# Kernel tuning notes

Measured on AMD Instinct MI355X. Metric: run time of the kernel, lower is better.

## Reference

```python
import jax, jax.numpy as jnp
import numpy as np
from jax import lax

INT8_NARROW = (-127.0, 127.0)   # brevitas Int8WeightPerTensorFloat (narrow range)
INT8_FULL = (-128.0, 127.0)     # brevitas Int8ActPerTensorFloat
INT32 = (-2.0**31, 2.0**31 - 1)


def _fake_quant(v, scale, qmin, qmax):
    # round-to-nearest, clip, dequant (per-tensor)
    return jnp.clip(jnp.round(v / scale), qmin, qmax) * scale


def _conv(x, w, stride):
    return lax.conv_general_dilated(
        x, w, window_strides=(stride, stride), padding=[(1, 1), (1, 1)],
        dimension_numbers=("NCHW", "OIHW", "NCHW"))


def setup_inputs() -> dict:
    key = jax.random.key(0)
    ks = jax.random.split(key, 5)
    B, Cin, Cout, H = 64, 256, 512, 28
    x = jax.random.normal(ks[0], (B, Cin, H, H), dtype=jnp.float32)
    w1 = jax.random.normal(ks[1], (Cout, Cin, 3, 3), dtype=jnp.float32) * 0.05
    b1 = jax.random.normal(ks[2], (Cout,), dtype=jnp.float32) * 0.01
    w2 = jax.random.normal(ks[3], (Cout, Cout, 3, 3), dtype=jnp.float32) * 0.05
    b2 = jax.random.normal(ks[4], (Cout,), dtype=jnp.float32) * 0.01
    return {
        "x": x, "w1": w1, "b1": b1, "w2": w2, "b2": b2,
        "in_scale": jnp.full((1,), 0.05, dtype=jnp.float32),
        "act1_scale": jnp.full((1,), 0.05, dtype=jnp.float32),
        "act2_scale": jnp.full((1,), 0.05, dtype=jnp.float32),
    }


def reference(x, w1, b1, w2, b2, in_scale, act1_scale, act2_scale):
    s_in = in_scale[0]
    s_a1 = act1_scale[0]
    s_a2 = act2_scale[0]

    # conv1: per-tensor int8 weight fake-quant (max-abs stats, narrow range)
    s_w1 = jnp.max(jnp.abs(w1)) / 127.0
    wq1 = _fake_quant(w1, s_w1, *INT8_NARROW)
    bq1 = _fake_quant(b1, s_in * s_w1, *INT32)  # Int32Bias: scale = in_scale*w_scale
    out = _conv(x, wq1, 2) + bq1[None, :, None, None]

    # act1: int8 activation fake-quant (learned per-tensor scale)
    out = _fake_quant(out, s_a1, *INT8_FULL)

    # conv2
    s_w2 = jnp.max(jnp.abs(w2)) / 127.0
    wq2 = _fake_quant(w2, s_w2, *INT8_NARROW)
    bq2 = _fake_quant(b2, s_a1 * s_w2, *INT32)
    out = _conv(out, wq2, 1) + bq2[None, :, None, None]

    # act2
    out = _fake_quant(out, s_a2, *INT8_FULL)
    return out
```

## Files before the change

kernel.cpp:

```cpp
#include <hip/hip_runtime.h>

typedef int i32x4 __attribute__((ext_vector_type(4)));

__device__ __forceinline__ void gl_lds16(const signed char* g, signed char* l) {
    __builtin_amdgcn_global_load_lds(
        (const __attribute__((address_space(1))) void*)g,
        (__attribute__((address_space(3))) void*)l, 16, 0, 0);
}

__device__ __forceinline__ i32x4 lds_read_b128(const signed char* p) {
    i32x4 r;
    const unsigned a = (unsigned)(uintptr_t)(const __attribute__((address_space(3))) signed char*)p;
    asm volatile("ds_read_b128 %0, %1" : "=v"(r) : "v"(a));
    return r;
}

#define XQ_SCALE 2048.0f
#define XQ_DELTA (1.0f / 2048.0f)

__device__ __forceinline__ float block_max256(const float* __restrict__ part, int base,
                                              float* __restrict__ sred) {
    float m = part[base + (threadIdx.x & 255)];
#pragma unroll
    for (int off = 32; off > 0; off >>= 1)
        m = fmaxf(m, __shfl_down(m, off));
    __syncthreads();
    if ((threadIdx.x & 63) == 0) sred[threadIdx.x >> 6] = m;
    __syncthreads();
    return fmaxf(fmaxf(sred[0], sred[1]), fmaxf(sred[2], sred[3]));
}

__global__ __launch_bounds__(256) void fused_pre_kernel(
    const float* __restrict__ x,
    const float* __restrict__ w1, const float* __restrict__ w2,
    float* __restrict__ part,
    signed char* __restrict__ xhi, signed char* __restrict__ xlo,
    signed char* __restrict__ act) {
    __shared__ float t[128][33];
    __shared__ float sred[4];
    const int blk = blockIdx.x;
    const int tid = threadIdx.x;
    const uint4 z = {0, 0, 0, 0};

    if (blk < 512) {
        const bool second = blk >= 256;
        const float* w = second ? w2 : w1;
        const int n4 = second ? 589824 : 294912;
        float m = 0.0f;
        for (int i = (blk & 255) * 256 + tid; i < n4; i += 65536) {
            float4 v = ((const float4*)w)[i];
            m = fmaxf(m, fmaxf(fmaxf(fabsf(v.x), fabsf(v.y)), fmaxf(fabsf(v.z), fabsf(v.w))));
        }
#pragma unroll
        for (int off = 32; off > 0; off >>= 1)
            m = fmaxf(m, __shfl_down(m, off));
        if ((tid & 63) == 0) sred[tid >> 6] = m;
        __syncthreads();
        if (tid == 0)
            part[blk] = fmaxf(fmaxf(sred[0], sred[1]), fmaxf(sred[2], sred[3]));
    } else if (blk < 976) {
        const int thr = (blk - 512) * 256 + tid;
        const int b = thr / (116 * 16);
        const int rr = thr - b * (116 * 16);
        const int p = rr >> 4;
        const int ch = rr & 15;
        int h, w;
        if (p < 30)      { h = 0;          w = p; }
        else if (p < 60) { h = 29;         w = p - 30; }
        else if (p < 88) { h = p - 60 + 1; w = 0; }
        else             { h = p - 88 + 1; w = 29; }
        const int off = (b * 900 + h * 30 + w) * 256 + ch * 16;
        *(uint4*)(xhi + off) = z;
        *(uint4*)(xlo + off) = z;
    } else if (blk < 1456) {
        const int thr = (blk - 976) * 256 + tid;
        const int b = thr / (60 * 32);
        const int rr = thr - b * (60 * 32);
        const int p = rr >> 5;
        const int ch = rr & 31;
        int h, w;
        if (p < 16)      { h = 0;          w = p; }
        else if (p < 32) { h = 15;         w = p - 16; }
        else if (p < 46) { h = p - 32 + 1; w = 0; }
        else             { h = p - 46 + 1; w = 15; }
        const int off = (b * 256 + h * 16 + w) * 512 + ch * 16;
        *(uint4*)(act + off) = z;
    } else {
        const int xb = blk - 1456;
        const int hwb = xb % 25;
        const int rest = xb / 25;
        const int cb = rest & 1;
        const int b = rest >> 1;
        const int c0 = cb * 128;
        const int hw0 = hwb * 32;
#pragma unroll
        for (int ci = 0; ci < 16; ++ci) {
            const int crow = (tid >> 5) + ci * 8;
            const int hw = hw0 + (tid & 31);
            float v = 0.0f;
            if (hw < 784) v = x[(b * 256 + c0 + crow) * 784 + hw];
            t[crow][tid & 31] = v;
        }
        __syncthreads();
        const int hw_l = tid >> 3;
        const int cg = (tid & 7) * 16;
        const int hw = hw0 + hw_l;
        if (hw < 784) {
            union { signed char c[16]; uint4 u; } ph, pl;
#pragma unroll
            for (int j = 0; j < 16; ++j) {
                const float v = t[cg + j][hw_l];
                int q = (int)rintf(v * XQ_SCALE);
                q = max(-16383, min(16383, q));
                ph.c[j] = (signed char)(q >> 7);
                pl.c[j] = (signed char)(q & 127);
            }
            const int r = hw / 28;
            const int o = (b * 900 + (r + 1) * 30 + (hw - r * 28) + 1) * 256 + c0 + cg;
            *(uint4*)&xhi[o] = ph.u;
            *(uint4*)&xlo[o] = pl.u;
        }
    }
}

__global__ __launch_bounds__(256) void prep_w_kernel(
    const float* __restrict__ w1, const float* __restrict__ w2,
    const float* __restrict__ b1, const float* __restrict__ b2,
    const float* __restrict__ part,
    const float* __restrict__ in_scale, const float* __restrict__ act1_scale,
    signed char* __restrict__ wq1, signed char* __restrict__ wq2,
    float* __restrict__ bq1, float* __restrict__ bq2,
    float* __restrict__ wmax) {
    __shared__ __align__(16) signed char sw[4608];
    __shared__ float sred[4];
    const int blk = blockIdx.x;
    const int tid = threadIdx.x;

    if (blk < 512) {
        const float inv_s = 127.0f / block_max256(part, 0, sred);
        const int n = blk;
#pragma unroll
        for (int rd = 0; rd < 9; ++rd) {
            const int idx = rd * 256 + tid;
            const float v = w1[n * 2304 + idx];
            float q = rintf(v * inv_s);
            q = fminf(fmaxf(q, -127.0f), 127.0f);
            const int cin = idx / 9;
            const int r = idx - cin * 9;
            sw[r * 256 + cin] = (signed char)(int)q;
        }
        __syncthreads();
        if (tid < 144) *(uint4*)&wq1[n * 2304 + tid * 16] = *(const uint4*)&sw[tid * 16];
    } else if (blk < 1024) {
        const float inv_s = 127.0f / block_max256(part, 256, sred);
        const int n = blk - 512;
#pragma unroll
        for (int rd = 0; rd < 18; ++rd) {
            const int idx = rd * 256 + tid;
            const float v = w2[n * 4608 + idx];
            float q = rintf(v * inv_s);
            q = fminf(fmaxf(q, -127.0f), 127.0f);
            const int cin = idx / 9;
            const int r = idx - cin * 9;
            sw[r * 512 + cin] = (signed char)(int)q;
        }
        __syncthreads();
        for (int o = tid; o < 288; o += 256)
            *(uint4*)&wq2[n * 4608 + o * 16] = *(const uint4*)&sw[o * 16];
    } else {
        const float m1 = block_max256(part, 0, sred);
        const float m2 = block_max256(part, 256, sred);
        if (tid == 0) { wmax[0] = m1; wmax[1] = m2; }
        for (int idx = tid; idx < 1024; idx += 256) {
            if (idx < 512) {
                const float s = (*in_scale) * (m1 * (1.0f / 127.0f));
                float q = rintf(b1[idx] / s);
                q = fminf(fmaxf(q, -2147483648.0f), 2147483648.0f);
                bq1[idx] = q * s;
            } else {
                const int j = idx - 512;
                const float s = (*act1_scale) * (m2 * (1.0f / 127.0f));
                float q = rintf(b2[j] / s);
                q = fminf(fmaxf(q, -2147483648.0f), 2147483648.0f);
                bq2[j] = q * s;
            }
        }
    }
}

template<int CIN, int STRIDE, int HP, int HOUT, bool SPLIT, bool FINAL>
__global__ __launch_bounds__(256, SPLIT ? 2 : 3) void conv_gemm_kernel(
    const signed char* __restrict__ Ahi,
    const signed char* __restrict__ Alo,
    const signed char* __restrict__ Wt,
    const float* __restrict__ bias,
    const float* __restrict__ wmax,
    const float* __restrict__ s_pre,
    const float* __restrict__ s_act,
    signed char* __restrict__ act_out,
    float* __restrict__ out_final)
{
    constexpr int K = 9 * CIN;
    constexpr int HW = HOUT * HOUT;
    constexpr int NIT = K / 128;
    constexpr int NC = SPLIT ? 8 : 6;
    constexpr int BUFSZ = SPLIT ? 32768 : 24576;
    constexpr int NB = SPLIT ? 4 : 2;

    __shared__ __align__(16) signed char smem[2 * BUFSZ];

    const int tid = threadIdx.x;
    const int lane = tid & 63;
    const int wv = tid >> 6;
    const int pair = wv >> 1;
    const int nh = wv & 1;
    const int quad = lane >> 4;
    const int l16 = lane & 15;
    const int m0 = blockIdx.y * 64;
    const int n0 = blockIdx.x * 128;

    const int lrow = lane >> 3;
    const int koff = ((lane & 7) ^ lrow) * 16;

    const signed char* srcb[NC];
    int dsto[NC];
    bool isA[NC];
    if constexpr (SPLIT) {
#pragma unroll
        for (int i = 0; i < NC; ++i) {
            const int g = wv * 8 + i;
            const int type = g >> 3;
            if (type >= 2) {
                const int c = g - 16;
                srcb[i] = Wt + (n0 + c * 8 + lrow) * K + koff;
                dsto[i] = 16384 + c * 1024;
                isA[i] = false;
            } else {
                const int c = g & 7;
                const int m = m0 + c * 8 + lrow;
                const int b = m / HW;
                const int rem = m - b * HW;
                const int oh = rem / HOUT;
                const int ow = rem - oh * HOUT;
                const int off = ((b * HP + oh * STRIDE) * HP + ow * STRIDE) * CIN + koff;
                srcb[i] = (type == 0 ? Ahi : Alo) + off;
                dsto[i] = type * 8192 + c * 1024;
                isA[i] = true;
            }
        }
    } else {
#pragma unroll
        for (int i = 0; i < NC; ++i) {
            const int g = wv * 6 + i;
            if (g < 8) {
                const int c = g;
                const int m = m0 + c * 8 + lrow;
                const int b = m / HW;
                const int rem = m - b * HW;
                const int oh = rem / HOUT;
                const int ow = rem - oh * HOUT;
                const int off = ((b * HP + oh * STRIDE) * HP + ow * STRIDE) * CIN + koff;
                srcb[i] = Ahi + off;
                dsto[i] = c * 1024;
                isA[i] = true;
            } else {
                const int c = g - 8;
                srcb[i] = Wt + (n0 + c * 8 + lrow) * K + koff;
                dsto[i] = 8192 + c * 1024;
                isA[i] = false;
            }
        }
    }

    const int aoff0 = SPLIT ? (pair * 8192) : 0;
    const int boff0 = SPLIT ? 16384 : 8192;
    const int nfix  = SPLIT ? (nh * 64) : (wv * 32);

    i32x4 acc[4][NB];
#pragma unroll
    for (int mi = 0; mi < 4; ++mi)
#pragma unroll
        for (int ni = 0; ni < NB; ++ni)
            acc[mi][ni] = i32x4{0, 0, 0, 0};

    auto STAGE = [&](int bo, int it) {
        const int k0 = it * 128;
        const int r9 = k0 / CIN;
        const int kh = r9 / 3;
        const int kw = r9 - kh * 3;
        const int ashift = (kh * HP + kw) * CIN + (k0 & (CIN - 1));
#pragma unroll
        for (int i = 0; i < NC; ++i)
            gl_lds16(srcb[i] + (isA[i] ? ashift : k0), &smem[bo + dsto[i]]);
    };

    auto LOADFRAGS = [&](int bo, i32x4 (&af)[2][4], i32x4 (&bf)[2][NB]) {
#pragma unroll
        for (int ks = 0; ks < 2; ++ks) {
#pragma unroll
            for (int mi = 0; mi < 4; ++mi) {
                const int row = mi * 16 + l16;
                const int sl = ((ks * 4 + quad) ^ (row & 7)) * 16;
                af[ks][mi] = lds_read_b128(&smem[bo + aoff0 + row * 128 + sl]);
            }
#pragma unroll
            for (int ni = 0; ni < NB; ++ni) {
                const int row = nfix + ni * 16 + l16;
                const int sl = ((ks * 4 + quad) ^ (row & 7)) * 16;
                bf[ks][ni] = lds_read_b128(&smem[bo + boff0 + row * 128 + sl]);
            }
        }
    };

    auto MFMAS = [&](i32x4 (&af)[2][4], i32x4 (&bf)[2][NB]) {
        __builtin_amdgcn_s_setprio(1);
#pragma unroll
        for (int ks = 0; ks < 2; ++ks)
#pragma unroll
            for (int mi = 0; mi < 4; ++mi)
#pragma unroll
                for (int ni = 0; ni < NB; ++ni)
                    acc[mi][ni] = __builtin_amdgcn_mfma_i32_16x16x64_i8(af[ks][mi], bf[ks][ni], acc[mi][ni], 0, 0, 0);
        __builtin_amdgcn_s_setprio(0);
    };

    auto WAIT_NC = [&]() {
        if constexpr (SPLIT) asm volatile("s_waitcnt vmcnt(8)" ::: "memory");
        else                 asm volatile("s_waitcnt vmcnt(6)" ::: "memory");
    };

    i32x4 af[2][4], bf[2][NB];

    STAGE(0, 0);
    STAGE(BUFSZ, 1);

    for (int it = 0; it < NIT - 2; it += 2) {
        WAIT_NC();
        __builtin_amdgcn_s_barrier();
        __builtin_amdgcn_sched_barrier(0);
        LOADFRAGS(0, af, bf);
        asm volatile("s_waitcnt lgkmcnt(0)" ::: "memory");
        __builtin_amdgcn_sched_barrier(0);
        __builtin_amdgcn_s_barrier();
        __builtin_amdgcn_sched_barrier(0);
        STAGE(0, it + 2);
        MFMAS(af, bf);

        WAIT_NC();
        __builtin_amdgcn_s_barrier();
        __builtin_amdgcn_sched_barrier(0);
        LOADFRAGS(BUFSZ, af, bf);
        asm volatile("s_waitcnt lgkmcnt(0)" ::: "memory");
        __builtin_amdgcn_sched_barrier(0);
        __builtin_amdgcn_s_barrier();
        __builtin_amdgcn_sched_barrier(0);
        if (it + 3 < NIT) STAGE(BUFSZ, it + 3);
        MFMAS(af, bf);
    }

    WAIT_NC();
    __builtin_amdgcn_s_barrier();
    __builtin_amdgcn_sched_barrier(0);
    LOADFRAGS(0, af, bf);
    asm volatile("s_waitcnt lgkmcnt(0)" ::: "memory");
    __builtin_amdgcn_sched_barrier(0);
    MFMAS(af, bf);

    asm volatile("s_waitcnt vmcnt(0)" ::: "memory");
    __builtin_amdgcn_s_barrier();
    __builtin_amdgcn_sched_barrier(0);
    LOADFRAGS(BUFSZ, af, bf);
    asm volatile("s_waitcnt lgkmcnt(0)" ::: "memory");
    __builtin_amdgcn_sched_barrier(0);
    MFMAS(af, bf);

    if constexpr (SPLIT) {
        __syncthreads();
        if (pair == 1) {
#pragma unroll
            for (int mi = 0; mi < 4; ++mi)
#pragma unroll
                for (int ni = 0; ni < 4; ++ni)
                    *(i32x4*)&smem[nh * 16384 + (mi * 4 + ni) * 1024 + lane * 16] = acc[mi][ni];
        }
        __syncthreads();
        if (pair == 1) return;
#pragma unroll
        for (int mi = 0; mi < 4; ++mi)
#pragma unroll
            for (int ni = 0; ni < 4; ++ni) {
                const i32x4 other = *(const i32x4*)&smem[nh * 16384 + (mi * 4 + ni) * 1024 + lane * 16];
                acc[mi][ni] = acc[mi][ni] * 128 + other;
            }
    }

    float alpha = (*wmax) * (1.0f / 127.0f);
    if (FINAL) alpha *= *s_pre;
    if (SPLIT) alpha *= XQ_DELTA;
    const float sact = *s_act;

    float bv[NB];
#pragma unroll
    for (int ni = 0; ni < NB; ++ni)
        bv[ni] = bias[n0 + nfix + ni * 16 + l16];

#pragma unroll
    for (int mi = 0; mi < 4; ++mi) {
#pragma unroll
        for (int i = 0; i < 4; ++i) {
            const int m = m0 + mi * 16 + quad * 4 + i;
            const int b = m / HW;
            const int rem = m - b * HW;
            const int oh = rem / HOUT;
            const int ow = rem - oh * HOUT;
#pragma unroll
            for (int ni = 0; ni < NB; ++ni) {
                const int col = n0 + nfix + ni * 16 + l16;
                const float v = (float)acc[mi][ni][i] * alpha + bv[ni];
                float q = rintf(v / sact);
                q = fminf(fmaxf(q, -128.0f), 127.0f);
                if (FINAL) {
                    out_final[(b * 512 + col) * HW + oh * HOUT + ow] = q * sact;
                } else {
                    act_out[(b * 256 + (oh + 1) * 16 + (ow + 1)) * 512 + col] = (signed char)(int)q;
                }
            }
        }
    }
}

extern "C" void kernel_launch(void* const* d_in, const int* in_sizes, int n_in,
                              void* d_out, int out_size, void* d_ws, size_t ws_size,
                              hipStream_t stream) {
    const float* x  = (const float*)d_in[0];
    const float* w1 = (const float*)d_in[1];
    const float* b1 = (const float*)d_in[2];
    const float* w2 = (const float*)d_in[3];
    const float* b2 = (const float*)d_in[4];
    const float* in_scale   = (const float*)d_in[5];
    const float* act1_scale = (const float*)d_in[6];
    const float* act2_scale = (const float*)d_in[7];
    float* out = (float*)d_out;

    char* ws = (char*)d_ws;
    float* part = (float*)(ws + 0);
    float* wmax = (float*)(ws + 2048);
    float* bq1 = (float*)(ws + 2176);
    float* bq2 = (float*)(ws + 4224);
    signed char* wq1 = (signed char*)(ws + 8192);
    signed char* wq2 = (signed char*)(ws + 1187840);
    signed char* xhi = (signed char*)(ws + 3547136);
    signed char* xlo = (signed char*)(ws + 18292736);
    signed char* act = (signed char*)(ws + 33038336);

    fused_pre_kernel<<<4656, 256, 0, stream>>>(x, w1, w2, part, xhi, xlo, act);

    prep_w_kernel<<<1025, 256, 0, stream>>>(w1, w2, b1, b2, part, in_scale, act1_scale,
                                            wq1, wq2, bq1, bq2, wmax);

    conv_gemm_kernel<256, 2, 30, 14, true, false><<<dim3(4, 196), 256, 0, stream>>>(
        xhi, xlo, wq1, bq1, wmax, act1_scale, act1_scale, act, nullptr);

    conv_gemm_kernel<512, 1, 16, 14, false, true><<<dim3(4, 196), 256, 0, stream>>>(
        act, nullptr, wq2, bq2, wmax + 1, act1_scale, act2_scale, nullptr, out);
}
```

Baseline: 234.1 us.

## Use 2-wave conv GEMM blocks with per-wave 64x64 tiles and in-register limb accumulation

```diff
diff --git a/kernel.cpp b/kernel.cpp
--- a/kernel.cpp
+++ b/kernel.cpp
@@ -189,7 +189,7 @@
 }
 
 template<int CIN, int STRIDE, int HP, int HOUT, bool SPLIT, bool FINAL>
-__global__ __launch_bounds__(256, SPLIT ? 2 : 3) void conv_gemm_kernel(
+__global__ __launch_bounds__(128, SPLIT ? 1 : 2) void conv_gemm_kernel(
     const signed char* __restrict__ Ahi,
     const signed char* __restrict__ Alo,
     const signed char* __restrict__ Wt,
@@ -203,21 +203,20 @@
     constexpr int K = 9 * CIN;
     constexpr int HW = HOUT * HOUT;
     constexpr int NIT = K / 128;
-    constexpr int NC = SPLIT ? 8 : 6;
+    constexpr int NC = SPLIT ? 16 : 12;
     constexpr int BUFSZ = SPLIT ? 32768 : 24576;
-    constexpr int NB = SPLIT ? 4 : 2;
+    constexpr int BOFF = SPLIT ? 16384 : 8192;
 
     __shared__ __align__(16) signed char smem[2 * BUFSZ];
 
     const int tid = threadIdx.x;
     const int lane = tid & 63;
     const int wv = tid >> 6;
-    const int pair = wv >> 1;
-    const int nh = wv & 1;
     const int quad = lane >> 4;
     const int l16 = lane & 15;
     const int m0 = blockIdx.y * 64;
     const int n0 = blockIdx.x * 128;
+    const int nfix = wv * 64;
 
     const int lrow = lane >> 3;
     const int koff = ((lane & 7) ^ lrow) * 16;
@@ -228,14 +227,9 @@
     if constexpr (SPLIT) {
 #pragma unroll
         for (int i = 0; i < NC; ++i) {
-            const int g = wv * 8 + i;
-            const int type = g >> 3;
-            if (type >= 2) {
-                const int c = g - 16;
-                srcb[i] = Wt + (n0 + c * 8 + lrow) * K + koff;
-                dsto[i] = 16384 + c * 1024;
-                isA[i] = false;
-            } else {
+            const int g = wv * 16 + i;
+            if (g < 16) {
+                const int limb = g >> 3;
                 const int c = g & 7;
                 const int m = m0 + c * 8 + lrow;
                 const int b = m / HW;
@@ -243,15 +237,20 @@
                 const int oh = rem / HOUT;
                 const int ow = rem - oh * HOUT;
                 const int off = ((b * HP + oh * STRIDE) * HP + ow * STRIDE) * CIN + koff;
-                srcb[i] = (type == 0 ? Ahi : Alo) + off;
-                dsto[i] = type * 8192 + c * 1024;
+                srcb[i] = (limb ? Alo : Ahi) + off;
+                dsto[i] = limb * 8192 + c * 1024;
                 isA[i] = true;
+            } else {
+                const int c = g - 16;
+                srcb[i] = Wt + (n0 + c * 8 + lrow) * K + koff;
+                dsto[i] = 16384 + c * 1024;
+                isA[i] = false;
             }
         }
     } else {
 #pragma unroll
         for (int i = 0; i < NC; ++i) {
-            const int g = wv * 6 + i;
+            const int g = wv * 12 + i;
             if (g < 8) {
                 const int c = g;
                 const int m = m0 + c * 8 + lrow;
@@ -272,16 +271,17 @@
         }
     }
 
-    const int aoff0 = SPLIT ? (pair * 8192) : 0;
-    const int boff0 = SPLIT ? 16384 : 8192;
-    const int nfix  = SPLIT ? (nh * 64) : (wv * 32);
-
-    i32x4 acc[4][NB];
+    i32x4 acc[4][4];
+    i32x4 acc2[4][4];
 #pragma unroll
     for (int mi = 0; mi < 4; ++mi)
 #pragma unroll
-        for (int ni = 0; ni < NB; ++ni)
+        for (int ni = 0; ni < 4; ++ni) {
             acc[mi][ni] = i32x4{0, 0, 0, 0};
+            if constexpr (SPLIT) acc2[mi][ni] = i32x4{0, 0, 0, 0};
+        }
+
+    i32x4 af[2][4], al[2][4], bf[2][4];
 
     auto STAGE = [&](int bo, int it) {
         const int k0 = it * 128;
@@ -294,42 +294,45 @@
             gl_lds16(srcb[i] + (isA[i] ? ashift : k0), &smem[bo + dsto[i]]);
     };
 
-    auto LOADFRAGS = [&](int bo, i32x4 (&af)[2][4], i32x4 (&bf)[2][NB]) {
+    auto LOADFRAGS = [&](int bo) {
 #pragma unroll
         for (int ks = 0; ks < 2; ++ks) {
 #pragma unroll
             for (int mi = 0; mi < 4; ++mi) {
                 const int row = mi * 16 + l16;
                 const int sl = ((ks * 4 + quad) ^ (row & 7)) * 16;
-                af[ks][mi] = lds_read_b128(&smem[bo + aoff0 + row * 128 + sl]);
-            }
-#pragma unroll
-            for (int ni = 0; ni < NB; ++ni) {
+                af[ks][mi] = lds_read_b128(&smem[bo + row * 128 + sl]);
+                if constexpr (SPLIT)
+                    al[ks][mi] = lds_read_b128(&smem[bo + 8192 + row * 128 + sl]);
+            }
+#pragma unroll
+            for (int ni = 0; ni < 4; ++ni) {
                 const int row = nfix + ni * 16 + l16;
                 const int sl = ((ks * 4 + quad) ^ (row & 7)) * 16;
-                bf[ks][ni] = lds_read_b128(&smem[bo + boff0 + row * 128 + sl]);
+                bf[ks][ni] = lds_read_b128(&smem[bo + BOFF + row * 128 + sl]);
             }
         }
     };
 
-    auto MFMAS = [&](i32x4 (&af)[2][4], i32x4 (&bf)[2][NB]) {
+    auto MFMAS = [&]() {
         __builtin_amdgcn_s_setprio(1);
 #pragma unroll
         for (int ks = 0; ks < 2; ++ks)
 #pragma unroll
             for (int mi = 0; mi < 4; ++mi)
 #pragma unroll
-                for (int ni = 0; ni < NB; ++ni)
+                for (int ni = 0; ni < 4; ++ni) {
                     acc[mi][ni] = __builtin_amdgcn_mfma_i32_16x16x64_i8(af[ks][mi], bf[ks][ni], acc[mi][ni], 0, 0, 0);
+                    if constexpr (SPLIT)
+                        acc2[mi][ni] = __builtin_amdgcn_mfma_i32_16x16x64_i8(al[ks][mi], bf[ks][ni], acc2[mi][ni], 0, 0, 0);
+                }
         __builtin_amdgcn_s_setprio(0);
     };
 
     auto WAIT_NC = [&]() {
-        if constexpr (SPLIT) asm volatile("s_waitcnt vmcnt(8)" ::: "memory");
-        else                 asm volatile("s_waitcnt vmcnt(6)" ::: "memory");
+        if constexpr (SPLIT) asm volatile("s_waitcnt vmcnt(16)" ::: "memory");
+        else                 asm volatile("s_waitcnt vmcnt(12)" ::: "memory");
     };
-
-    i32x4 af[2][4], bf[2][NB];
 
     STAGE(0, 0);
     STAGE(BUFSZ, 1);
@@ -338,60 +341,48 @@
         WAIT_NC();
         __builtin_amdgcn_s_barrier();
         __builtin_amdgcn_sched_barrier(0);
-        LOADFRAGS(0, af, bf);
+        LOADFRAGS(0);
         asm volatile("s_waitcnt lgkmcnt(0)" ::: "memory");
         __builtin_amdgcn_sched_barrier(0);
         __builtin_amdgcn_s_barrier();
         __builtin_amdgcn_sched_barrier(0);
         STAGE(0, it + 2);
-        MFMAS(af, bf);
+        MFMAS();
 
         WAIT_NC();
         __builtin_amdgcn_s_barrier();
         __builtin_amdgcn_sched_barrier(0);
-        LOADFRAGS(BUFSZ, af, bf);
+        LOADFRAGS(BUFSZ);
         asm volatile("s_waitcnt lgkmcnt(0)" ::: "memory");
         __builtin_amdgcn_sched_barrier(0);
         __builtin_amdgcn_s_barrier();
         __builtin_amdgcn_sched_barrier(0);
         if (it + 3 < NIT) STAGE(BUFSZ, it + 3);
-        MFMAS(af, bf);
+        MFMAS();
     }
 
     WAIT_NC();
     __builtin_amdgcn_s_barrier();
     __builtin_amdgcn_sched_barrier(0);
-    LOADFRAGS(0, af, bf);
+    LOADFRAGS(0);
     asm volatile("s_waitcnt lgkmcnt(0)" ::: "memory");
     __builtin_amdgcn_sched_barrier(0);
-    MFMAS(af, bf);
+    MFMAS();
 
     asm volatile("s_waitcnt vmcnt(0)" ::: "memory");
     __builtin_amdgcn_s_barrier();
     __builtin_amdgcn_sched_barrier(0);
-    LOADFRAGS(BUFSZ, af, bf);
+    LOADFRAGS(BUFSZ);
     asm volatile("s_waitcnt lgkmcnt(0)" ::: "memory");
     __builtin_amdgcn_sched_barrier(0);
-    MFMAS(af, bf);
+    MFMAS();
 
     if constexpr (SPLIT) {
-        __syncthreads();
-        if (pair == 1) {
-#pragma unroll
-            for (int mi = 0; mi < 4; ++mi)
-#pragma unroll
-                for (int ni = 0; ni < 4; ++ni)
-                    *(i32x4*)&smem[nh * 16384 + (mi * 4 + ni) * 1024 + lane * 16] = acc[mi][ni];
-        }
-        __syncthreads();
-        if (pair == 1) return;
 #pragma unroll
         for (int mi = 0; mi < 4; ++mi)
 #pragma unroll
-            for (int ni = 0; ni < 4; ++ni) {
-                const i32x4 other = *(const i32x4*)&smem[nh * 16384 + (mi * 4 + ni) * 1024 + lane * 16];
-                acc[mi][ni] = acc[mi][ni] * 128 + other;
-            }
+            for (int ni = 0; ni < 4; ++ni)
+                acc[mi][ni] = acc[mi][ni] * 128 + acc2[mi][ni];
     }
 
     float alpha = (*wmax) * (1.0f / 127.0f);
@@ -399,9 +390,9 @@
     if (SPLIT) alpha *= XQ_DELTA;
     const float sact = *s_act;
 
-    float bv[NB];
-#pragma unroll
-    for (int ni = 0; ni < NB; ++ni)
+    float bv[4];
+#pragma unroll
+    for (int ni = 0; ni < 4; ++ni)
         bv[ni] = bias[n0 + nfix + ni * 16 + l16];
 
 #pragma unroll
@@ -414,7 +405,7 @@
             const int oh = rem / HOUT;
             const int ow = rem - oh * HOUT;
 #pragma unroll
-            for (int ni = 0; ni < NB; ++ni) {
+            for (int ni = 0; ni < 4; ++ni) {
                 const int col = n0 + nfix + ni * 16 + l16;
                 const float v = (float)acc[mi][ni][i] * alpha + bv[ni];
                 float q = rintf(v / sact);
@@ -458,9 +449,9 @@
     prep_w_kernel<<<1025, 256, 0, stream>>>(w1, w2, b1, b2, part, in_scale, act1_scale,
                                             wq1, wq2, bq1, bq2, wmax);
 
-    conv_gemm_kernel<256, 2, 30, 14, true, false><<<dim3(4, 196), 256, 0, stream>>>(
+    conv_gemm_kernel<256, 2, 30, 14, true, false><<<dim3(4, 196), 128, 0, stream>>>(
         xhi, xlo, wq1, bq1, wmax, act1_scale, act1_scale, act, nullptr);
 
-    conv_gemm_kernel<512, 1, 16, 14, false, true><<<dim3(4, 196), 256, 0, stream>>>(
+    conv_gemm_kernel<512, 1, 16, 14, false, true><<<dim3(4, 196), 128, 0, stream>>>(
         act, nullptr, wq2, bq2, wmax + 1, act1_scale, act2_scale, nullptr, out);
 }
```

After: 244.5 us. +4.4%, slower.
